# Kernel optimization log

Measured on AMD Instinct MI355X. Metric: run time of the kernel, lower is better.

## Reference

```python
import jax, jax.numpy as jnp
import numpy as np

HEADS = 6
WS = 16          # window_size
OWS = 24         # overlap_win_size
DIM = 192
TABLE = (WS + OWS - 1) ** 2  # 1521


def setup_inputs() -> dict:
    key = jax.random.key(0)
    k1, k2, k3, k4, k5, k6 = jax.random.split(key, 6)
    b = 256
    nq = WS * WS          # 256
    n = OWS * OWS         # 576
    x_q = jax.random.normal(k1, (b, nq, DIM), dtype=jnp.float32)
    x_kv = jax.random.normal(k2, (b, n, DIM), dtype=jnp.float32)
    rpi = jax.random.randint(k3, (nq, n), 0, TABLE, dtype=jnp.int64)
    Wq = jax.random.normal(k4, (DIM, DIM), dtype=jnp.float32) * 0.02
    Wkv = jax.random.normal(k5, (2 * DIM, DIM), dtype=jnp.float32) * 0.02
    bias_table = jax.random.normal(k6, (TABLE, HEADS), dtype=jnp.float32) * 0.02
    return {"x_q": x_q, "x_kv": x_kv, "rpi": rpi, "Wq": Wq, "Wkv": Wkv, "bias_table": bias_table}


def reference(x_q, x_kv, rpi, Wq, Wkv, bias_table):
    b, nq, dim = x_q.shape
    n = x_kv.shape[1]
    hd = dim // HEADS
    scale = hd ** (-0.5)

    # projections (torch Linear: y = x @ W^T)
    q = (x_q @ Wq.T).reshape(b, nq, HEADS, hd).transpose(0, 2, 1, 3)      # b h nq d
    kv = x_kv @ Wkv.T                                                    # b n 2*dim
    k, v = jnp.split(kv, 2, axis=-1)
    k = k.reshape(b, n, HEADS, hd).transpose(0, 2, 1, 3)                  # b h n d
    v = v.reshape(b, n, HEADS, hd).transpose(0, 2, 1, 3)                  # b h n d

    attn = scale * jnp.einsum('bhqd,bhkd->bhqk', q, k)                    # b h nq n

    # gathered relative-position bias: table[rpi] -> (nq, n, h)
    rpb = bias_table[rpi.reshape(-1)].reshape(nq, n, HEADS)
    # nq < n branch in source: permute(2, 0, 1) -> (h, nq, n)
    rpb = rpb.transpose(2, 0, 1)

    attn = jax.nn.softmax(attn + rpb[None], axis=-1)
    out = jnp.einsum('bhqk,bhkd->bhqd', attn, v)                          # b h nq d
    out = out.transpose(0, 2, 1, 3).reshape(b, nq, dim)
    return out
```

## Files before the change

### kernel.cpp

```cpp
#include <hip/hip_runtime.h>
#include <cstdint>

typedef unsigned short u16;
typedef short s16x8 __attribute__((ext_vector_type(8)));
typedef float f32x4 __attribute__((ext_vector_type(4)));
typedef float f32x16 __attribute__((ext_vector_type(16)));

#if __has_builtin(__builtin_amdgcn_exp2f)
#define EXP2(x) __builtin_amdgcn_exp2f(x)
#else
#define EXP2(x) __expf((x)*0.6931471805599453f)
#endif

__device__ __forceinline__ u16 f2bf(float x) {
  uint32_t u = __builtin_bit_cast(uint32_t, x);
  u += 0x7FFFu + ((u >> 16) & 1u);
  return (u16)(u >> 16);
}
__device__ __forceinline__ float bf2f(u16 v) {
  return __builtin_bit_cast(float, (uint32_t)v << 16);
}
__device__ __forceinline__ uint32_t pk_bf16(float lo, float hi) {
  uint32_t ul = __builtin_bit_cast(uint32_t, lo);
  uint32_t uh = __builtin_bit_cast(uint32_t, hi);
  ul += 0x7FFFu + ((ul >> 16) & 1u);
  uh += 0x7FFFu + ((uh >> 16) & 1u);
  return __builtin_amdgcn_perm(uh, ul, 0x07060302u);
}
__device__ __forceinline__ f32x4 mfma16(s16x8 a, s16x8 b, f32x4 c) {
  return __builtin_amdgcn_mfma_f32_16x16x32_bf16(a, b, c, 0, 0, 0);
}
__device__ __forceinline__ f32x16 mfma32(s16x8 a, s16x8 b, f32x16 c) {
  return __builtin_amdgcn_mfma_f32_32x32x16_bf16(a, b, c, 0, 0, 0);
}
__device__ __forceinline__ s16x8 ld_frag(const u16* p) {
  uint4 v = *(const uint4*)p;
  return __builtin_bit_cast(s16x8, v);
}

__global__ void prep_w(const float* __restrict__ Wq, const float* __restrict__ Wkv,
                       u16* __restrict__ wqs, u16* __restrict__ wkvs) {
  int tid = blockIdx.x * 256 + threadIdx.x;
  if (tid >= 13824) return;
  bool isQ = tid < 4608;
  int id = isQ ? tid : tid - 4608;
  int lane = id & 63, fk = id >> 6;
  int kk = fk % 6, fb = fk / 6;
  int f = fb * 16 + (lane & 15), k0 = kk * 32 + ((lane >> 4) << 3);
  const float* src = (isQ ? Wq : Wkv) + (size_t)f * 192 + k0;
  const float sc = isQ ? 0.2550348583f : 1.0f;
  float4 a = ((const float4*)src)[0], b = ((const float4*)src)[1];
  uint4 o;
  o.x = pk_bf16(a.x * sc, a.y * sc); o.y = pk_bf16(a.z * sc, a.w * sc);
  o.z = pk_bf16(b.x * sc, b.y * sc); o.w = pk_bf16(b.z * sc, b.w * sc);
  *(uint4*)&(isQ ? wqs : wkvs)[(size_t)id * 8] = o;
}

__global__ void build_rpb(const int* __restrict__ rpi, const float* __restrict__ table,
                          u16* __restrict__ rpb) {
  int n = blockIdx.x, q = threadIdx.x;
  int idx = rpi[q * 576 + n] * 6;
#pragma unroll
  for (int hh = 0; hh < 6; ++hh)
    rpb[(size_t)hh * 147456 + n * 256 + q] = f2bf(table[idx + hh] * 1.4426950409f);
}

#define LDA 200
template <int NC, int MODE>
__device__ __forceinline__ void proj_body(const float* __restrict__ A,
                                          const u16* __restrict__ W,
                                          u16* __restrict__ outQ, u16* __restrict__ outK,
                                          u16* __restrict__ outV, int blk,
                                          u16* __restrict__ lA) {
  const int t = threadIdx.x, lane = t & 63, w = t >> 6, c = lane & 15, hi = lane >> 4;
  const int mbase0 = blk << 6;
  {
    const int row = t >> 2, cq = t & 3;
    const float* src = A + (size_t)(mbase0 + row) * 192 + (cq << 2);
    u16* dst = lA + row * LDA + (cq << 2);
#pragma unroll
    for (int i = 0; i < 12; ++i) {
      float4 v = *(const float4*)(src + (i << 4));
      uint2 p;
      p.x = pk_bf16(v.x, v.y);
      p.y = pk_bf16(v.z, v.w);
      *(uint2*)(dst + (i << 4)) = p;
    }
  }
  __syncthreads();
  s16x8 af[6];
  const u16* lrow = lA + (w * 16 + c) * LDA;
#pragma unroll
  for (int kk = 0; kk < 6; ++kk)
    af[kk] = ld_frag(lrow + (kk << 5) + (hi << 3));

  constexpr int TOT = NC * 6;
  const int m = mbase0 + (w << 4) + c;
  s16x8 w0[4], w1[4], w2[4];
#pragma unroll
  for (int nb = 0; nb < 4; ++nb)
    w0[nb] = ld_frag(&W[((size_t)((nb * 6) * 64 + lane)) * 8]);
#pragma unroll
  for (int nb = 0; nb < 4; ++nb)
    w1[nb] = ld_frag(&W[((size_t)((nb * 6 + 1) * 64 + lane)) * 8]);
  f32x4 acc[4];
#pragma unroll
  for (int nb = 0; nb < 4; ++nb) acc[nb] = f32x4{0.f, 0.f, 0.f, 0.f};
#pragma unroll
  for (int s = 0; s < TOT; ++s) {
    const int nc = s / 6, kk = s % 6;
    if (s + 2 < TOT) {
      const int nc2 = (s + 2) / 6, kk2 = (s + 2) % 6;
#pragma unroll
      for (int nb = 0; nb < 4; ++nb)
        w2[nb] = ld_frag(&W[((size_t)((((nc2 << 2) + nb) * 6 + kk2) * 64 + lane)) * 8]);
    }
#pragma unroll
    for (int nb = 0; nb < 4; ++nb) acc[nb] = mfma16(w0[nb], af[kk], acc[nb]);
    if (kk == 5) {
#pragma unroll
      for (int nb = 0; nb < 4; ++nb) {
        int fb = (nc << 6) + (nb << 4) + (hi << 2);
        uint2 pv;
        pv.x = pk_bf16(acc[nb][0], acc[nb][1]);
        pv.y = pk_bf16(acc[nb][2], acc[nb][3]);
        if (MODE == 0) {
          int b = m >> 8, q = m & 255, hh = fb >> 5, d = fb & 31;
          *(uint2*)&outQ[((((size_t)(b * 6 + hh)) << 8) + q) * 32 + d] = pv;
        } else {
          int b = m / 576, tok = m - b * 576;
          if (fb >= 192) {
            int f2 = fb - 192, hh = f2 >> 5, d = f2 & 31;
            *(uint2*)&outV[(((size_t)(b * 6 + hh)) * 576 + tok) * 32 + d] = pv;
          } else {
            int hh = fb >> 5, dd = fb & 31;
            int half = dd >> 4, uu = (dd >> 3) & 1, e0 = dd & 7;
            int kt = tok >> 5, lt = tok & 31;
            *(uint2*)&outK[(size_t)((b * 6 + hh) * 18 + kt) * 1024 +
                           half * 512 + uu * 256 + lt * 8 + e0] = pv;
          }
        }
        acc[nb] = f32x4{0.f, 0.f, 0.f, 0.f};
      }
    }
#pragma unroll
    for (int nb = 0; nb < 4; ++nb) { w0[nb] = w1[nb]; w1[nb] = w2[nb]; }
  }
}

__launch_bounds__(256)
__global__ void proj_all(const float* __restrict__ xq, const float* __restrict__ xkv,
                         const u16* __restrict__ wqs, const u16* __restrict__ wkvs,
                         u16* __restrict__ Qws, u16* __restrict__ Kws,
                         u16* __restrict__ Vws) {
  __shared__ __align__(16) u16 lA[64 * LDA];
  int blk = blockIdx.x;
  if (blk < 1024) proj_body<3, 0>(xq, wqs, Qws, nullptr, nullptr, blk, lA);
  else            proj_body<6, 1>(xkv, wkvs, nullptr, Kws, Vws, blk - 1024, lA);
}

#define VSTR 600
__launch_bounds__(512)
__global__ void attn(const u16* __restrict__ Qws, const u16* __restrict__ Kws,
                     const u16* __restrict__ Vws, const u16* __restrict__ rpb,
                     float* __restrict__ out) {
  __shared__ __align__(16) u16 Vt[32 * VSTR];
  const int bh = blockIdx.x, b = bh / 6, h = bh - b * 6;
  const size_t kvbase = (size_t)bh * 576 * 32;
  const int t = threadIdx.x;
  for (int key = t; key < 576; key += 512) {
    int kk = key & 31, k15 = kk & 15;
    int p = ((kk >> 4) << 4) | (((k15 >> 2) & 1) << 3) | ((k15 >> 3) << 2) | (k15 & 3);
    int col = ((key >> 5) << 5) + p;
    const uint4* src = (const uint4*)&Vws[kvbase + (size_t)key * 32];
    uint4 r[4] = {src[0], src[1], src[2], src[3]};
    const u16* vs = (const u16*)r;
#pragma unroll
    for (int d = 0; d < 32; ++d) Vt[d * VSTR + col] = vs[d];
  }
  const int lane = t & 63, l31 = lane & 31, u = lane >> 5, w = t >> 6;
  const int qg = (w << 5) + l31;
  s16x8 qf[2];
#pragma unroll
  for (int m = 0; m < 2; ++m)
    qf[m] = ld_frag(&Qws[((size_t)bh * 256 + qg) * 32 + (m << 4) + (u << 3)]);
  __syncthreads();
  f32x16 oacc;
#pragma unroll
  for (int r = 0; r < 16; ++r) oacc[r] = 0.f;
  float psum = 0.f;
  const u16* kfb = Kws + (size_t)bh * 18432 + (size_t)lane * 8;
  const u16* bpu = rpb + (size_t)h * 147456 + ((size_t)u << 10) + qg;
  s16x8 kA[2], kB[2];
  ushort bb[2][16];
  kA[0] = ld_frag(kfb);        kB[0] = ld_frag(kfb + 512);
  kA[1] = ld_frag(kfb + 1024); kB[1] = ld_frag(kfb + 1536);
#pragma unroll
  for (int r = 0; r < 16; ++r) {
    const int C = ((r >> 2) << 3) + (r & 3);
    bb[0][r] = bpu[(size_t)C << 8];
    bb[1][r] = bpu[(size_t)(32 + C) << 8];
  }
#pragma unroll 2
  for (int kt = 0; kt < 18; ++kt) {
    const int k0 = kt << 5, cur = kt & 1;
    s16x8 vf0 = ld_frag(&Vt[l31 * VSTR + k0 + (u << 3)]);
    s16x8 vf1 = ld_frag(&Vt[l31 * VSTR + k0 + 16 + (u << 3)]);
    f32x16 st;
#pragma unroll
    for (int r = 0; r < 16; ++r) st[r] = 0.f;
    st = mfma32(kA[cur], qf[0], st);
    st = mfma32(kB[cur], qf[1], st);
    ushort bc[16];
#pragma unroll
    for (int r = 0; r < 16; ++r) bc[r] = bb[cur][r];
    if (kt < 16) {
      kA[cur] = ld_frag(kfb + (size_t)(kt + 2) * 1024);
      kB[cur] = ld_frag(kfb + (size_t)(kt + 2) * 1024 + 512);
#pragma unroll
      for (int r = 0; r < 16; ++r) {
        const int C = ((r >> 2) << 3) + (r & 3);
        bb[cur][r] = bpu[(size_t)((kt + 2) * 32 + C) << 8];
      }
    }
    float e[16];
#pragma unroll
    for (int r = 0; r < 16; ++r)
      e[r] = EXP2(st[r] + bf2f(bc[r]));
    psum += (((e[0] + e[1]) + (e[2] + e[3])) + ((e[4] + e[5]) + (e[6] + e[7]))) +
            (((e[8] + e[9]) + (e[10] + e[11])) + ((e[12] + e[13]) + (e[14] + e[15])));
    uint4 pa, pb;
    pa.x = pk_bf16(e[0], e[1]);   pa.y = pk_bf16(e[2], e[3]);
    pa.z = pk_bf16(e[4], e[5]);   pa.w = pk_bf16(e[6], e[7]);
    pb.x = pk_bf16(e[8], e[9]);   pb.y = pk_bf16(e[10], e[11]);
    pb.z = pk_bf16(e[12], e[13]); pb.w = pk_bf16(e[14], e[15]);
    s16x8 pf0 = __builtin_bit_cast(s16x8, pa);
    s16x8 pf1 = __builtin_bit_cast(s16x8, pb);
    oacc = mfma32(vf0, pf0, oacc);
    oacc = mfma32(vf1, pf1, oacc);
  }
  float tot = psum + __shfl_xor(psum, 32);
  float rs = 1.0f / tot;
  float* op = out + ((size_t)b * 256 + qg) * 192 + h * 32 + (u << 2);
#pragma unroll
  for (int g = 0; g < 4; ++g) {
    float4 o;
    o.x = oacc[(g << 2) + 0] * rs; o.y = oacc[(g << 2) + 1] * rs;
    o.z = oacc[(g << 2) + 2] * rs; o.w = oacc[(g << 2) + 3] * rs;
    *(float4*)(op + (g << 3)) = o;
  }
}

extern "C" void kernel_launch(void* const* d_in, const int* in_sizes, int n_in,
                              void* d_out, int out_size, void* d_ws, size_t ws_size,
                              hipStream_t stream) {
  const float* x_q   = (const float*)d_in[0];
  const float* x_kv  = (const float*)d_in[1];
  const int*   rpi   = (const int*)d_in[2];
  const float* Wq    = (const float*)d_in[3];
  const float* Wkv   = (const float*)d_in[4];
  const float* table = (const float*)d_in[5];
  float* out = (float*)d_out;

  char* ws = (char*)d_ws;
  u16* wqs  = (u16*)(ws);
  u16* wkvs = (u16*)(ws + 73728);
  u16* rpb  = (u16*)(ws + 221184);
  u16* Qws  = (u16*)(ws + 1990656);
  u16* Kws  = (u16*)(ws + 27156480);
  u16* Vws  = (u16*)(ws + 83779584);

  prep_w<<<54, 256, 0, stream>>>(Wq, Wkv, wqs, wkvs);
  build_rpb<<<576, 256, 0, stream>>>(rpi, table, rpb);
  proj_all<<<3328, 256, 0, stream>>>(x_q, x_kv, wqs, wkvs, Qws, Kws, Vws);
  attn<<<1536, 512, 0, stream>>>(Qws, Kws, Vws, rpb, out);
}
```

Measured before the change: 348.1 us.

## Store bias in per-thread fragment order and double rows per projection block

The relative-position bias buffer is rebuilt in the exact order each attention thread consumes it. The attention loop can then fetch its 16 bias values with two 16-byte vector loads instead of 16 scattered scalar loads per key tile. Separately, the projection kernel now handles 128 rows per block with a fragment-ordered LDS layout, so each weight fragment is reused across two row groups and half as many blocks are launched. In exchange it uses more registers and LDS per projection block.

```diff
diff --git a/kernel.cpp b/kernel.cpp
--- a/kernel.cpp
+++ b/kernel.cpp
@@ -58,93 +58,115 @@
 
 __global__ void build_rpb(const int* __restrict__ rpi, const float* __restrict__ table,
                           u16* __restrict__ rpb) {
-  int n = blockIdx.x, q = threadIdx.x;
-  int idx = rpi[q * 576 + n] * 6;
-#pragma unroll
-  for (int hh = 0; hh < 6; ++hh)
-    rpb[(size_t)hh * 147456 + n * 256 + q] = f2bf(table[idx + hh] * 1.4426950409f);
-}
-
-#define LDA 200
+  const int bi = blockIdx.x;
+  const int h = bi / 18, kt = bi - h * 18;
+  const int t = threadIdx.x, lane = t & 63, w = t >> 6;
+  const int u = lane >> 5, l31 = lane & 31;
+  const int q = (w << 5) + l31;
+  const int n0 = (kt << 5) + (u << 2);
+  u16 vals[16];
+#pragma unroll
+  for (int g = 0; g < 4; ++g) {
+    int4 id4 = *(const int4*)&rpi[q * 576 + n0 + (g << 3)];
+    vals[(g << 2) + 0] = f2bf(table[id4.x * 6 + h] * 1.4426950409f);
+    vals[(g << 2) + 1] = f2bf(table[id4.y * 6 + h] * 1.4426950409f);
+    vals[(g << 2) + 2] = f2bf(table[id4.z * 6 + h] * 1.4426950409f);
+    vals[(g << 2) + 3] = f2bf(table[id4.w * 6 + h] * 1.4426950409f);
+  }
+  uint4* dst = (uint4*)&rpb[((size_t)bi * 512 + t) * 16];
+  dst[0] = *(uint4*)&vals[0];
+  dst[1] = *(uint4*)&vals[8];
+}
+
 template <int NC, int MODE>
 __device__ __forceinline__ void proj_body(const float* __restrict__ A,
                                           const u16* __restrict__ W,
                                           u16* __restrict__ outQ, u16* __restrict__ outK,
                                           u16* __restrict__ outV, int blk,
-                                          u16* __restrict__ lA) {
+                                          u16* __restrict__ lAf) {
   const int t = threadIdx.x, lane = t & 63, w = t >> 6, c = lane & 15, hi = lane >> 4;
-  const int mbase0 = blk << 6;
-  {
-    const int row = t >> 2, cq = t & 3;
+  const int mbase0 = blk << 7;
+#pragma unroll
+  for (int p = 0; p < 2; ++p) {
+    const int row = (p << 6) + (t >> 2), cq = t & 3;
+    const int fr = row >> 4, cc = row & 15;
     const float* src = A + (size_t)(mbase0 + row) * 192 + (cq << 2);
-    u16* dst = lA + row * LDA + (cq << 2);
+    const int e0 = (cq & 1) << 2;
 #pragma unroll
     for (int i = 0; i < 12; ++i) {
       float4 v = *(const float4*)(src + (i << 4));
-      uint2 p;
-      p.x = pk_bf16(v.x, v.y);
-      p.y = pk_bf16(v.z, v.w);
-      *(uint2*)(dst + (i << 4)) = p;
+      const int kk = i >> 1, h2 = ((i & 1) << 1) + (cq >> 1);
+      uint2 pv;
+      pv.x = pk_bf16(v.x, v.y);
+      pv.y = pk_bf16(v.z, v.w);
+      *(uint2*)&lAf[((((fr * 6 + kk) << 6) + (h2 << 4) + cc) << 3) + e0] = pv;
     }
   }
   __syncthreads();
-  s16x8 af[6];
-  const u16* lrow = lA + (w * 16 + c) * LDA;
-#pragma unroll
-  for (int kk = 0; kk < 6; ++kk)
-    af[kk] = ld_frag(lrow + (kk << 5) + (hi << 3));
+  s16x8 af[2][6];
+#pragma unroll
+  for (int rg = 0; rg < 2; ++rg)
+#pragma unroll
+    for (int kk = 0; kk < 6; ++kk)
+      af[rg][kk] = ld_frag(&lAf[((((((w << 1) + rg) * 6 + kk) << 6) + lane) << 3)]);
 
   constexpr int TOT = NC * 6;
-  const int m = mbase0 + (w << 4) + c;
-  s16x8 w0[4], w1[4], w2[4];
-#pragma unroll
-  for (int nb = 0; nb < 4; ++nb)
-    w0[nb] = ld_frag(&W[((size_t)((nb * 6) * 64 + lane)) * 8]);
-#pragma unroll
-  for (int nb = 0; nb < 4; ++nb)
-    w1[nb] = ld_frag(&W[((size_t)((nb * 6 + 1) * 64 + lane)) * 8]);
-  f32x4 acc[4];
-#pragma unroll
-  for (int nb = 0; nb < 4; ++nb) acc[nb] = f32x4{0.f, 0.f, 0.f, 0.f};
+  s16x8 wB[3][4];
+#pragma unroll
+  for (int s0 = 0; s0 < 2; ++s0) {
+#pragma unroll
+    for (int nb = 0; nb < 4; ++nb)
+      wB[s0][nb] = ld_frag(&W[((size_t)((nb * 6 + s0) * 64 + lane)) * 8]);
+  }
+  f32x4 acc[2][4];
+#pragma unroll
+  for (int rg = 0; rg < 2; ++rg)
+#pragma unroll
+    for (int nb = 0; nb < 4; ++nb) acc[rg][nb] = f32x4{0.f, 0.f, 0.f, 0.f};
 #pragma unroll
   for (int s = 0; s < TOT; ++s) {
     const int nc = s / 6, kk = s % 6;
     if (s + 2 < TOT) {
-      const int nc2 = (s + 2) / 6, kk2 = (s + 2) % 6;
+      const int s2 = s + 2, nc2 = s2 / 6, kk2 = s2 % 6;
 #pragma unroll
       for (int nb = 0; nb < 4; ++nb)
-        w2[nb] = ld_frag(&W[((size_t)((((nc2 << 2) + nb) * 6 + kk2) * 64 + lane)) * 8]);
-    }
-#pragma unroll
-    for (int nb = 0; nb < 4; ++nb) acc[nb] = mfma16(w0[nb], af[kk], acc[nb]);
+        wB[s2 % 3][nb] = ld_frag(&W[((size_t)((((nc2 << 2) + nb) * 6 + kk2) * 64 + lane)) * 8]);
+    }
+#pragma unroll
+    for (int rg = 0; rg < 2; ++rg)
+#pragma unroll
+      for (int nb = 0; nb < 4; ++nb)
+        acc[rg][nb] = mfma16(wB[s % 3][nb], af[rg][kk], acc[rg][nb]);
     if (kk == 5) {
 #pragma unroll
-      for (int nb = 0; nb < 4; ++nb) {
-        int fb = (nc << 6) + (nb << 4) + (hi << 2);
-        uint2 pv;
-        pv.x = pk_bf16(acc[nb][0], acc[nb][1]);
-        pv.y = pk_bf16(acc[nb][2], acc[nb][3]);
-        if (MODE == 0) {
-          int b = m >> 8, q = m & 255, hh = fb >> 5, d = fb & 31;
-          *(uint2*)&outQ[((((size_t)(b * 6 + hh)) << 8) + q) * 32 + d] = pv;
-        } else {
-          int b = m / 576, tok = m - b * 576;
-          if (fb >= 192) {
-            int f2 = fb - 192, hh = f2 >> 5, d = f2 & 31;
-            *(uint2*)&outV[(((size_t)(b * 6 + hh)) * 576 + tok) * 32 + d] = pv;
+      for (int rg = 0; rg < 2; ++rg) {
+        const int m = mbase0 + (w << 5) + (rg << 4) + c;
+#pragma unroll
+        for (int nb = 0; nb < 4; ++nb) {
+          int fb = (nc << 6) + (nb << 4) + (hi << 2);
+          uint2 pv;
+          pv.x = pk_bf16(acc[rg][nb][0], acc[rg][nb][1]);
+          pv.y = pk_bf16(acc[rg][nb][2], acc[rg][nb][3]);
+          if (MODE == 0) {
+            int b = m >> 8, q = m & 255, hh = fb >> 5, d = fb & 31;
+            *(uint2*)&outQ[((((size_t)(b * 6 + hh)) << 8) + q) * 32 + d] = pv;
           } else {
-            int hh = fb >> 5, dd = fb & 31;
-            int half = dd >> 4, uu = (dd >> 3) & 1, e0 = dd & 7;
-            int kt = tok >> 5, lt = tok & 31;
-            *(uint2*)&outK[(size_t)((b * 6 + hh) * 18 + kt) * 1024 +
-                           half * 512 + uu * 256 + lt * 8 + e0] = pv;
+            int b = m / 576, tok = m - b * 576;
+            if (fb >= 192) {
+              int f2 = fb - 192, hh = f2 >> 5, d = f2 & 31;
+              *(uint2*)&outV[(((size_t)(b * 6 + hh)) * 576 + tok) * 32 + d] = pv;
+            } else {
+              int hh = fb >> 5, dd = fb & 31;
+              int half = dd >> 4, uu = (dd >> 3) & 1, e0 = dd & 7;
+              int ktt = tok >> 5, lt = tok & 31;
+              *(uint2*)&outK[(size_t)((b * 6 + hh) * 18 + ktt) * 1024 +
+                             half * 512 + uu * 256 + lt * 8 + e0] = pv;
+            }
           }
+          acc[rg][nb] = f32x4{0.f, 0.f, 0.f, 0.f};
         }
-        acc[nb] = f32x4{0.f, 0.f, 0.f, 0.f};
       }
     }
-#pragma unroll
-    for (int nb = 0; nb < 4; ++nb) { w0[nb] = w1[nb]; w1[nb] = w2[nb]; }
   }
 }
 
@@ -153,10 +175,10 @@
                          const u16* __restrict__ wqs, const u16* __restrict__ wkvs,
                          u16* __restrict__ Qws, u16* __restrict__ Kws,
                          u16* __restrict__ Vws) {
-  __shared__ __align__(16) u16 lA[64 * LDA];
+  __shared__ __align__(16) u16 lAf[24576];
   int blk = blockIdx.x;
-  if (blk < 1024) proj_body<3, 0>(xq, wqs, Qws, nullptr, nullptr, blk, lA);
-  else            proj_body<6, 1>(xkv, wkvs, nullptr, Kws, Vws, blk - 1024, lA);
+  if (blk < 512) proj_body<3, 0>(xq, wqs, Qws, nullptr, nullptr, blk, lAf);
+  else           proj_body<6, 1>(xkv, wkvs, nullptr, Kws, Vws, blk - 512, lAf);
 }
 
 #define VSTR 600
@@ -190,17 +212,13 @@
   for (int r = 0; r < 16; ++r) oacc[r] = 0.f;
   float psum = 0.f;
   const u16* kfb = Kws + (size_t)bh * 18432 + (size_t)lane * 8;
-  const u16* bpu = rpb + (size_t)h * 147456 + ((size_t)u << 10) + qg;
+  const u16* bp0 = rpb + (size_t)h * 147456 + (size_t)t * 16;
   s16x8 kA[2], kB[2];
-  ushort bb[2][16];
+  uint4 bA[2], bB[2];
   kA[0] = ld_frag(kfb);        kB[0] = ld_frag(kfb + 512);
   kA[1] = ld_frag(kfb + 1024); kB[1] = ld_frag(kfb + 1536);
-#pragma unroll
-  for (int r = 0; r < 16; ++r) {
-    const int C = ((r >> 2) << 3) + (r & 3);
-    bb[0][r] = bpu[(size_t)C << 8];
-    bb[1][r] = bpu[(size_t)(32 + C) << 8];
-  }
+  bA[0] = *(const uint4*)(bp0);        bB[0] = *(const uint4*)(bp0 + 8);
+  bA[1] = *(const uint4*)(bp0 + 8192); bB[1] = *(const uint4*)(bp0 + 8192 + 8);
 #pragma unroll 2
   for (int kt = 0; kt < 18; ++kt) {
     const int k0 = kt << 5, cur = kt & 1;
@@ -211,22 +229,22 @@
     for (int r = 0; r < 16; ++r) st[r] = 0.f;
     st = mfma32(kA[cur], qf[0], st);
     st = mfma32(kB[cur], qf[1], st);
-    ushort bc[16];
-#pragma unroll
-    for (int r = 0; r < 16; ++r) bc[r] = bb[cur][r];
+    uint4 bAc = bA[cur], bBc = bB[cur];
     if (kt < 16) {
       kA[cur] = ld_frag(kfb + (size_t)(kt + 2) * 1024);
       kB[cur] = ld_frag(kfb + (size_t)(kt + 2) * 1024 + 512);
-#pragma unroll
-      for (int r = 0; r < 16; ++r) {
-        const int C = ((r >> 2) << 3) + (r & 3);
-        bb[cur][r] = bpu[(size_t)((kt + 2) * 32 + C) << 8];
-      }
-    }
+      bA[cur] = *(const uint4*)(bp0 + (size_t)(kt + 2) * 8192);
+      bB[cur] = *(const uint4*)(bp0 + (size_t)(kt + 2) * 8192 + 8);
+    }
+    const u16* b0 = (const u16*)&bAc;
+    const u16* b1 = (const u16*)&bBc;
     float e[16];
 #pragma unroll
-    for (int r = 0; r < 16; ++r)
-      e[r] = EXP2(st[r] + bf2f(bc[r]));
+    for (int r = 0; r < 8; ++r)
+      e[r] = EXP2(st[r] + bf2f(b0[r]));
+#pragma unroll
+    for (int r = 8; r < 16; ++r)
+      e[r] = EXP2(st[r] + bf2f(b1[r - 8]));
     psum += (((e[0] + e[1]) + (e[2] + e[3])) + ((e[4] + e[5]) + (e[6] + e[7]))) +
             (((e[8] + e[9]) + (e[10] + e[11])) + ((e[12] + e[13]) + (e[14] + e[15])));
     uint4 pa, pb;
@@ -271,7 +289,7 @@
   u16* Vws  = (u16*)(ws + 83779584);
 
   prep_w<<<54, 256, 0, stream>>>(Wq, Wkv, wqs, wkvs);
-  build_rpb<<<576, 256, 0, stream>>>(rpi, table, rpb);
-  proj_all<<<3328, 256, 0, stream>>>(x_q, x_kv, wqs, wkvs, Qws, Kws, Vws);
+  build_rpb<<<108, 512, 0, stream>>>(rpi, table, rpb);
+  proj_all<<<1664, 256, 0, stream>>>(x_q, x_kv, wqs, wkvs, Qws, Kws, Vws);
   attn<<<1536, 512, 0, stream>>>(Qws, Kws, Vws, rpb, out);
 }
```

After: 360.6 us. +3.6%, slower.
